# Optimization experiments

Measured on AMD Instinct MI355X. Metric: run time of the kernel, lower is better.

## Reference

```python
import jax, jax.numpy as jnp
import numpy as np

EMB = 1024
HEADS = 16
HEAD_SIZE = EMB // HEADS  # 64
B, T = 2, 2048


def setup_inputs() -> dict:
    key = jax.random.key(0)
    k1, k2, k3 = jax.random.split(key, 3)
    x = jax.random.normal(k1, (B, T, EMB), dtype=jnp.float32)
    # scale weights like typical init to keep logits sane
    w_qkv = jax.random.normal(k2, (EMB, 3 * EMB), dtype=jnp.float32) * (EMB ** -0.5)
    w_proj = jax.random.normal(k3, (EMB, EMB), dtype=jnp.float32) * (EMB ** -0.5)
    b_proj = jnp.zeros((EMB,), dtype=jnp.float32)
    return {"x": x, "w_qkv": w_qkv, "w_proj": w_proj, "b_proj": b_proj}


def reference(x, w_qkv, w_proj, b_proj):
    Bb, Tt, C = x.shape
    qkv = x @ w_qkv  # [B,T,3C]
    q, k, v = jnp.split(qkv, 3, axis=-1)
    # [B,H,T,hs]
    q = q.reshape(Bb, Tt, HEADS, HEAD_SIZE).transpose(0, 2, 1, 3)
    k = k.reshape(Bb, Tt, HEADS, HEAD_SIZE).transpose(0, 2, 1, 3)
    v = v.reshape(Bb, Tt, HEADS, HEAD_SIZE).transpose(0, 2, 1, 3)
    scale = HEAD_SIZE ** -0.5
    wei = jnp.einsum('bhqd,bhkd->bhqk', q, k) * scale  # [B,H,T,T]
    causal = jnp.tril(jnp.ones((Tt, Tt), dtype=bool))
    wei = jnp.where(causal, wei, -jnp.inf)
    wei = jax.nn.softmax(wei, axis=-1)
    out = jnp.einsum('bhqk,bhkd->bhqd', wei, v)  # [B,H,T,hs]
    out = out.transpose(0, 2, 1, 3).reshape(Bb, Tt, C)
    out = out @ w_proj + b_proj
    return out
```

## Files before the change

### kernel.cpp

```cpp
#include <hip/hip_runtime.h>
#include <hip/hip_bf16.h>

typedef __attribute__((ext_vector_type(8))) short short8;
typedef __attribute__((ext_vector_type(4))) float floatx4;

#define MFMA16(a, b, c) __builtin_amdgcn_mfma_f32_16x16x32_bf16((a), (b), (c), 0, 0, 0)
#define GLOBAL_AS __attribute__((address_space(1)))
#define LDS_AS __attribute__((address_space(3)))

__device__ __forceinline__ unsigned short f2bf(float x) {
  union { float f; unsigned u; } v; v.f = x;
  unsigned r = v.u + 0x7FFFu + ((v.u >> 16) & 1u);
  return (unsigned short)(r >> 16);
}

__device__ __forceinline__ short8 ld8(const unsigned short* p) {
  return *reinterpret_cast<const short8*>(p);
}

__device__ __forceinline__ void async_cp16(const unsigned short* g, unsigned short* l) {
  __builtin_amdgcn_global_load_lds((const GLOBAL_AS void*)g, (LDS_AS void*)l, 16, 0, 0);
}

__global__ void k_f32_to_bf16(const float* __restrict__ in,
                              unsigned short* __restrict__ out, int n4) {
  int i = blockIdx.x * blockDim.x + threadIdx.x;
  if (i >= n4) return;
  float4 f = reinterpret_cast<const float4*>(in)[i];
  union { unsigned short u[4]; unsigned long long v; } o;
  o.u[0] = f2bf(f.x); o.u[1] = f2bf(f.y); o.u[2] = f2bf(f.z); o.u[3] = f2bf(f.w);
  reinterpret_cast<unsigned long long*>(out)[i] = o.v;
}

__global__ void k_transpose_bf16(const float* __restrict__ in,
                                 unsigned short* __restrict__ out, int R, int C) {
  __shared__ float tile[64][65];
  int c0 = blockIdx.x * 64, r0 = blockIdx.y * 64;
  int tx = threadIdx.x, ty = threadIdx.y;
  for (int i = ty; i < 64; i += 4)
    tile[i][tx] = in[(size_t)(r0 + i) * C + c0 + tx];
  __syncthreads();
  for (int i = ty; i < 64; i += 4)
    out[(size_t)(c0 + i) * R + r0 + tx] = f2bf(tile[tx][i]);
}

__global__ void k_vtrans(const unsigned short* __restrict__ qkvb,
                         unsigned short* __restrict__ vT) {
  const int T = 2048, LD = 3072;
  __shared__ unsigned short tile[64][72];
  int bh = blockIdx.y, b = bh >> 4, h = bh & 15;
  int t0 = blockIdx.x * 64;
  int tx = threadIdx.x, ty = threadIdx.y;
  const unsigned short* src = qkvb + (size_t)b * T * LD + 2048 + h * 64;
  for (int i = ty; i < 64; i += 4)
    tile[i][tx] = src[(size_t)(t0 + i) * LD + tx];
  __syncthreads();
  unsigned short* dst = vT + (size_t)bh * 64 * T;
  for (int i = ty; i < 64; i += 4)
    dst[(size_t)i * T + t0 + tx] = tile[tx][i];
}

template <int OUT_BF16, int HAS_BIAS>
__global__ __launch_bounds__(256) void k_gemm_bt(
    const unsigned short* __restrict__ A, const unsigned short* __restrict__ Bt,
    void* __restrict__ Cout, const float* __restrict__ bias, int M, int N, int K) {
  __shared__ unsigned short As[128][64];
  __shared__ unsigned short Bs[128][64];
  int tid = threadIdx.x;
  int w = tid >> 6, lane = tid & 63, quad = lane >> 4, l16 = lane & 15;
  int wy = w >> 1, wx = w & 1;
  int rowB = blockIdx.y * 128, colB = blockIdx.x * 128;
  int srcRow = lane >> 3;
  int srcCol = (((lane & 7) ^ (srcRow & 7)) << 3);

  floatx4 acc[4][4];
  floatx4 zero4 = {0.f, 0.f, 0.f, 0.f};
#pragma unroll
  for (int mi = 0; mi < 4; ++mi)
#pragma unroll
    for (int ni = 0; ni < 4; ++ni) acc[mi][ni] = zero4;

  for (int kt = 0; kt < K; kt += 64) {
    __syncthreads();
#pragma unroll
    for (int i = 0; i < 4; ++i) {
      int r0 = w * 32 + i * 8;
      async_cp16(&A[(size_t)(rowB + r0 + srcRow) * K + kt + srcCol], &As[r0][0]);
      async_cp16(&Bt[(size_t)(colB + r0 + srcRow) * K + kt + srcCol], &Bs[r0][0]);
    }
    __syncthreads();
#pragma unroll
    for (int kh = 0; kh < 2; ++kh) {
      short8 af[4], bf_[4];
#pragma unroll
      for (int mi = 0; mi < 4; ++mi)
        af[mi] = ld8(&As[wy * 64 + mi * 16 + l16][((kh * 4 + quad) ^ (l16 & 7)) << 3]);
#pragma unroll
      for (int ni = 0; ni < 4; ++ni)
        bf_[ni] = ld8(&Bs[wx * 64 + ni * 16 + l16][((kh * 4 + quad) ^ (l16 & 7)) << 3]);
#pragma unroll
      for (int mi = 0; mi < 4; ++mi)
#pragma unroll
        for (int ni = 0; ni < 4; ++ni)
          acc[mi][ni] = MFMA16(af[mi], bf_[ni], acc[mi][ni]);
    }
  }

#pragma unroll
  for (int mi = 0; mi < 4; ++mi) {
    int row = rowB + wy * 64 + mi * 16 + quad * 4;
#pragma unroll
    for (int ni = 0; ni < 4; ++ni) {
      int col = colB + wx * 64 + ni * 16 + l16;
      float bv = HAS_BIAS ? bias[col] : 0.f;
#pragma unroll
      for (int r = 0; r < 4; ++r) {
        float val = acc[mi][ni][r] + bv;
        if (OUT_BF16)
          ((unsigned short*)Cout)[(size_t)(row + r) * N + col] = f2bf(val);
        else
          ((float*)Cout)[(size_t)(row + r) * N + col] = val;
      }
    }
  }
}

__global__ __launch_bounds__(256) void k_attn(
    const unsigned short* __restrict__ qkv, const unsigned short* __restrict__ vT,
    unsigned short* __restrict__ attn_out) {
  const int T = 2048, LD = 3072;
  __shared__ unsigned short Kt[64][72];
  __shared__ unsigned short Vt[64][72];
  __shared__ unsigned short Pt[4][2][16][72];

  int bh = blockIdx.y, b = bh >> 4, h = bh & 15;
  int ip = blockIdx.x;
  int tid = threadIdx.x, w = tid >> 6, lane = tid & 63;
  int quad = lane >> 4, l16 = lane & 15;

  const unsigned short* Qp = qkv + (size_t)b * T * LD + h * 64;
  const unsigned short* Kp = Qp + 1024;
  const unsigned short* Vp = vT + (size_t)bh * 64 * T;

  const int q0s[2] = {ip * 64, (31 - ip) * 64};
  const int lastkt[2] = {ip, 31 - ip};
  int nt = 32 - ip;

  short8 aq[2][2];
#pragma unroll
  for (int m = 0; m < 2; ++m) {
    const unsigned short* qrow = Qp + (size_t)(q0s[m] + w * 16 + l16) * LD + quad * 8;
    aq[m][0] = ld8(qrow);
    aq[m][1] = ld8(qrow + 32);
  }

  short8 ones8;
  {
    unsigned short o = 0x3F80;
#pragma unroll
    for (int j = 0; j < 8; ++j) ones8[j] = (short)o;
  }

  const float cscale = 0.125f * 1.44269504f;
  floatx4 o_acc[2][4], l_acc[2];
  floatx4 zero4 = {0.f, 0.f, 0.f, 0.f};
#pragma unroll
  for (int m = 0; m < 2; ++m) {
    l_acc[m] = zero4;
#pragma unroll
    for (int nd = 0; nd < 4; ++nd) o_acc[m][nd] = zero4;
  }

  int stR = tid >> 3, stC = (tid & 7) << 3;

  short8 kreg[2], vreg[2];
#pragma unroll
  for (int j = 0; j < 2; ++j) {
    int r = stR + j * 32;
    kreg[j] = ld8(&Kp[(size_t)r * LD + stC]);
    vreg[j] = ld8(&Vp[(size_t)r * T + stC]);
  }

  for (int kt = 0; kt < nt; ++kt) {
    __syncthreads();
#pragma unroll
    for (int j = 0; j < 2; ++j) {
      int r = stR + j * 32;
      *reinterpret_cast<short8*>(&Kt[r][stC]) = kreg[j];
      *reinterpret_cast<short8*>(&Vt[r][stC]) = vreg[j];
    }
    __syncthreads();

    if (kt + 1 < nt) {
      int key0n = (kt + 1) * 64;
#pragma unroll
      for (int j = 0; j < 2; ++j) {
        int r = stR + j * 32;
        kreg[j] = ld8(&Kp[(size_t)(key0n + r) * LD + stC]);
        vreg[j] = ld8(&Vp[(size_t)r * T + key0n + stC]);
      }
    }

    int key0 = kt * 64;
    bool act0 = (kt <= lastkt[0]);

    floatx4 st[2][4];
#pragma unroll
    for (int kt4 = 0; kt4 < 4; ++kt4) {
      short8 ak0 = ld8(&Kt[kt4 * 16 + l16][quad * 8]);
      short8 ak1 = ld8(&Kt[kt4 * 16 + l16][32 + quad * 8]);
      st[1][kt4] = MFMA16(ak0, aq[1][0], zero4);
      st[1][kt4] = MFMA16(ak1, aq[1][1], st[1][kt4]);
      if (act0) {
        st[0][kt4] = MFMA16(ak0, aq[0][0], zero4);
        st[0][kt4] = MFMA16(ak1, aq[0][1], st[0][kt4]);
      }
    }

#pragma unroll
    for (int m = 0; m < 2; ++m) {
      if (m == 0 && !act0) continue;
      if (kt == lastkt[m]) {
        int qlane = q0s[m] + w * 16 + l16;
#pragma unroll
        for (int kt4 = 0; kt4 < 4; ++kt4)
#pragma unroll
          for (int r = 0; r < 4; ++r)
            if (key0 + kt4 * 16 + quad * 4 + r > qlane) st[m][kt4][r] = -1e30f;
      }
#pragma unroll
      for (int kt4 = 0; kt4 < 4; ++kt4) {
        unsigned u[4];
#pragma unroll
        for (int r = 0; r < 4; ++r)
          u[r] = __float_as_uint(
              __builtin_amdgcn_exp2f(fmaf(st[m][kt4][r], cscale, -16.f)));
        unsigned lo = __builtin_amdgcn_perm(u[1], u[0], 0x07060302u);
        unsigned hi = __builtin_amdgcn_perm(u[3], u[2], 0x07060302u);
        unsigned long long pv = ((unsigned long long)hi << 32) | lo;
        *reinterpret_cast<unsigned long long*>(
            &Pt[w][m][l16][kt4 * 16 + quad * 4]) = pv;
      }
    }

    short8 pa[2][2];
    pa[1][0] = ld8(&Pt[w][1][l16][quad * 8]);
    pa[1][1] = ld8(&Pt[w][1][l16][32 + quad * 8]);
    if (act0) {
      pa[0][0] = ld8(&Pt[w][0][l16][quad * 8]);
      pa[0][1] = ld8(&Pt[w][0][l16][32 + quad * 8]);
    }
#pragma unroll
    for (int nd = 0; nd < 4; ++nd) {
      short8 bv0 = ld8(&Vt[nd * 16 + l16][quad * 8]);
      short8 bv1 = ld8(&Vt[nd * 16 + l16][32 + quad * 8]);
      o_acc[1][nd] = MFMA16(pa[1][0], bv0, o_acc[1][nd]);
      o_acc[1][nd] = MFMA16(pa[1][1], bv1, o_acc[1][nd]);
      if (act0) {
        o_acc[0][nd] = MFMA16(pa[0][0], bv0, o_acc[0][nd]);
        o_acc[0][nd] = MFMA16(pa[0][1], bv1, o_acc[0][nd]);
      }
    }
    l_acc[1] = MFMA16(pa[1][0], ones8, l_acc[1]);
    l_acc[1] = MFMA16(pa[1][1], ones8, l_acc[1]);
    if (act0) {
      l_acc[0] = MFMA16(pa[0][0], ones8, l_acc[0]);
      l_acc[0] = MFMA16(pa[0][1], ones8, l_acc[0]);
    }
  }

#pragma unroll
  for (int m = 0; m < 2; ++m)
#pragma unroll
    for (int nd = 0; nd < 4; ++nd)
#pragma unroll
      for (int r = 0; r < 4; ++r) {
        int q = q0s[m] + w * 16 + quad * 4 + r;
        int d = nd * 16 + l16;
        attn_out[(size_t)(b * T + q) * 1024 + h * 64 + d] =
            f2bf(o_acc[m][nd][r] / l_acc[m][r]);
      }
}

extern "C" void kernel_launch(void* const* d_in, const int* in_sizes, int n_in,
                              void* d_out, int out_size, void* d_ws, size_t ws_size,
                              hipStream_t stream) {
  const float* x = (const float*)d_in[0];
  const float* w_qkv = (const float*)d_in[1];
  const float* w_proj = (const float*)d_in[2];
  const float* b_proj = (const float*)d_in[3];
  float* out = (float*)d_out;

  char* ws = (char*)d_ws;
  unsigned short* xb     = (unsigned short*)(ws);
  unsigned short* wqkvT  = (unsigned short*)(ws + (size_t)(8  << 20));
  unsigned short* wprojT = (unsigned short*)(ws + (size_t)(14 << 20));
  unsigned short* qkvb   = (unsigned short*)(ws + (size_t)(16 << 20));
  unsigned short* attnb  = (unsigned short*)(ws + (size_t)(40 << 20));
  unsigned short* vTb    = xb;

  k_f32_to_bf16<<<4096, 256, 0, stream>>>(x, xb, (4096 * 1024) / 4);
  dim3 tb(64, 4);
  k_transpose_bf16<<<dim3(3072 / 64, 1024 / 64), tb, 0, stream>>>(w_qkv, wqkvT, 1024, 3072);
  k_transpose_bf16<<<dim3(1024 / 64, 1024 / 64), tb, 0, stream>>>(w_proj, wprojT, 1024, 1024);
  k_gemm_bt<1, 0><<<dim3(3072 / 128, 4096 / 128), 256, 0, stream>>>(
      xb, wqkvT, qkvb, nullptr, 4096, 3072, 1024);
  k_vtrans<<<dim3(2048 / 64, 2 * 16), tb, 0, stream>>>(qkvb, vTb);
  k_attn<<<dim3(16, 2 * 16), 256, 0, stream>>>(qkvb, vTb, attnb);
  k_gemm_bt<0, 1><<<dim3(1024 / 128, 4096 / 128), 256, 0, stream>>>(
      attnb, wprojT, out, b_proj, 4096, 1024, 1024);
}
```

Baseline: 200.3 us.

## Double-buffer K/V tiles in LDS to drop one barrier per iteration

Turns the K and V shared-memory tiles into two-slot buffers. Each iteration writes the next tile into the other slot and issues global loads two tiles ahead, so only one __syncthreads per iteration remains. It also pads the P staging rows from 72 to 76 elements, likely to change the LDS bank mapping. The cost is more LDS per block, which may lower occupancy, and a deeper register prefetch.

```diff
diff --git a/kernel.cpp b/kernel.cpp
--- a/kernel.cpp
+++ b/kernel.cpp
@@ -129,9 +129,9 @@
     const unsigned short* __restrict__ qkv, const unsigned short* __restrict__ vT,
     unsigned short* __restrict__ attn_out) {
   const int T = 2048, LD = 3072;
-  __shared__ unsigned short Kt[64][72];
-  __shared__ unsigned short Vt[64][72];
-  __shared__ unsigned short Pt[4][2][16][72];
+  __shared__ unsigned short Kt[2][64][72];
+  __shared__ unsigned short Vt[2][64][72];
+  __shared__ unsigned short Pt[4][2][16][76];
 
   int bh = blockIdx.y, b = bh >> 4, h = bh & 15;
   int ip = blockIdx.x;
@@ -180,24 +180,39 @@
     kreg[j] = ld8(&Kp[(size_t)r * LD + stC]);
     vreg[j] = ld8(&Vp[(size_t)r * T + stC]);
   }
-
-  for (int kt = 0; kt < nt; ++kt) {
-    __syncthreads();
+#pragma unroll
+  for (int j = 0; j < 2; ++j) {
+    int r = stR + j * 32;
+    *reinterpret_cast<short8*>(&Kt[0][r][stC]) = kreg[j];
+    *reinterpret_cast<short8*>(&Vt[0][r][stC]) = vreg[j];
+  }
+  if (nt > 1) {
 #pragma unroll
     for (int j = 0; j < 2; ++j) {
       int r = stR + j * 32;
-      *reinterpret_cast<short8*>(&Kt[r][stC]) = kreg[j];
-      *reinterpret_cast<short8*>(&Vt[r][stC]) = vreg[j];
-    }
-    __syncthreads();
-
+      kreg[j] = ld8(&Kp[(size_t)(64 + r) * LD + stC]);
+      vreg[j] = ld8(&Vp[(size_t)r * T + 64 + stC]);
+    }
+  }
+  __syncthreads();
+
+  for (int kt = 0; kt < nt; ++kt) {
+    int cur = kt & 1;
     if (kt + 1 < nt) {
-      int key0n = (kt + 1) * 64;
 #pragma unroll
       for (int j = 0; j < 2; ++j) {
         int r = stR + j * 32;
-        kreg[j] = ld8(&Kp[(size_t)(key0n + r) * LD + stC]);
-        vreg[j] = ld8(&Vp[(size_t)r * T + key0n + stC]);
+        *reinterpret_cast<short8*>(&Kt[1 - cur][r][stC]) = kreg[j];
+        *reinterpret_cast<short8*>(&Vt[1 - cur][r][stC]) = vreg[j];
+      }
+      if (kt + 2 < nt) {
+        int key0n = (kt + 2) * 64;
+#pragma unroll
+        for (int j = 0; j < 2; ++j) {
+          int r = stR + j * 32;
+          kreg[j] = ld8(&Kp[(size_t)(key0n + r) * LD + stC]);
+          vreg[j] = ld8(&Vp[(size_t)r * T + key0n + stC]);
+        }
       }
     }
 
@@ -207,8 +222,8 @@
     floatx4 st[2][4];
 #pragma unroll
     for (int kt4 = 0; kt4 < 4; ++kt4) {
-      short8 ak0 = ld8(&Kt[kt4 * 16 + l16][quad * 8]);
-      short8 ak1 = ld8(&Kt[kt4 * 16 + l16][32 + quad * 8]);
+      short8 ak0 = ld8(&Kt[cur][kt4 * 16 + l16][quad * 8]);
+      short8 ak1 = ld8(&Kt[cur][kt4 * 16 + l16][32 + quad * 8]);
       st[1][kt4] = MFMA16(ak0, aq[1][0], zero4);
       st[1][kt4] = MFMA16(ak1, aq[1][1], st[1][kt4]);
       if (act0) {
@@ -252,8 +267,8 @@
     }
 #pragma unroll
     for (int nd = 0; nd < 4; ++nd) {
-      short8 bv0 = ld8(&Vt[nd * 16 + l16][quad * 8]);
-      short8 bv1 = ld8(&Vt[nd * 16 + l16][32 + quad * 8]);
+      short8 bv0 = ld8(&Vt[cur][nd * 16 + l16][quad * 8]);
+      short8 bv1 = ld8(&Vt[cur][nd * 16 + l16][32 + quad * 8]);
       o_acc[1][nd] = MFMA16(pa[1][0], bv0, o_acc[1][nd]);
       o_acc[1][nd] = MFMA16(pa[1][1], bv1, o_acc[1][nd]);
       if (act0) {
@@ -267,6 +282,8 @@
       l_acc[0] = MFMA16(pa[0][0], ones8, l_acc[0]);
       l_acc[0] = MFMA16(pa[0][1], ones8, l_acc[0]);
     }
+
+    __syncthreads();
   }
 
 #pragma unroll
```

New measurement: 210.9 us. 5.3% more time.

## Replace paired causal q-block scheduling with one q-block per workgroup

Applied to the files above, without the earlier changes.

The attention kernel previously gave each workgroup two query blocks (ip and 31-ip) so every workgroup did equal causal work while sharing each K/V tile load. It now launches 32 workgroups per head, each handling a single query block, with the heaviest blocks scheduled first via the reversed block index. This doubles parallelism (1024 workgroups instead of 512) and halves per-wave registers, but it loses the K/V reuse across two query blocks, so total K/V loads go up and per-workgroup work becomes unbalanced. The P staging buffer is shrunk and re-padded to 76 columns.

```diff
diff --git a/kernel.cpp b/kernel.cpp
--- a/kernel.cpp
+++ b/kernel.cpp
@@ -131,10 +131,10 @@
   const int T = 2048, LD = 3072;
   __shared__ unsigned short Kt[64][72];
   __shared__ unsigned short Vt[64][72];
-  __shared__ unsigned short Pt[4][2][16][72];
+  __shared__ unsigned short Pt[4][16][76];
 
   int bh = blockIdx.y, b = bh >> 4, h = bh & 15;
-  int ip = blockIdx.x;
+  int qblk = 31 - blockIdx.x;
   int tid = threadIdx.x, w = tid >> 6, lane = tid & 63;
   int quad = lane >> 4, l16 = lane & 15;
 
@@ -142,16 +142,14 @@
   const unsigned short* Kp = Qp + 1024;
   const unsigned short* Vp = vT + (size_t)bh * 64 * T;
 
-  const int q0s[2] = {ip * 64, (31 - ip) * 64};
-  const int lastkt[2] = {ip, 31 - ip};
-  int nt = 32 - ip;
-
-  short8 aq[2][2];
-#pragma unroll
-  for (int m = 0; m < 2; ++m) {
-    const unsigned short* qrow = Qp + (size_t)(q0s[m] + w * 16 + l16) * LD + quad * 8;
-    aq[m][0] = ld8(qrow);
-    aq[m][1] = ld8(qrow + 32);
+  int q0 = qblk * 64;
+  int nt = qblk + 1;
+
+  short8 aq[2];
+  {
+    const unsigned short* qrow = Qp + (size_t)(q0 + w * 16 + l16) * LD + quad * 8;
+    aq[0] = ld8(qrow);
+    aq[1] = ld8(qrow + 32);
   }
 
   short8 ones8;
@@ -162,14 +160,11 @@
   }
 
   const float cscale = 0.125f * 1.44269504f;
-  floatx4 o_acc[2][4], l_acc[2];
+  floatx4 o_acc[4], l_acc;
   floatx4 zero4 = {0.f, 0.f, 0.f, 0.f};
-#pragma unroll
-  for (int m = 0; m < 2; ++m) {
-    l_acc[m] = zero4;
-#pragma unroll
-    for (int nd = 0; nd < 4; ++nd) o_acc[m][nd] = zero4;
-  }
+  l_acc = zero4;
+#pragma unroll
+  for (int nd = 0; nd < 4; ++nd) o_acc[nd] = zero4;
 
   int stR = tid >> 3, stC = (tid & 7) << 3;
 
@@ -202,84 +197,61 @@
     }
 
     int key0 = kt * 64;
-    bool act0 = (kt <= lastkt[0]);
-
-    floatx4 st[2][4];
+
+    floatx4 st[4];
 #pragma unroll
     for (int kt4 = 0; kt4 < 4; ++kt4) {
       short8 ak0 = ld8(&Kt[kt4 * 16 + l16][quad * 8]);
       short8 ak1 = ld8(&Kt[kt4 * 16 + l16][32 + quad * 8]);
-      st[1][kt4] = MFMA16(ak0, aq[1][0], zero4);
-      st[1][kt4] = MFMA16(ak1, aq[1][1], st[1][kt4]);
-      if (act0) {
-        st[0][kt4] = MFMA16(ak0, aq[0][0], zero4);
-        st[0][kt4] = MFMA16(ak1, aq[0][1], st[0][kt4]);
-      }
-    }
-
-#pragma unroll
-    for (int m = 0; m < 2; ++m) {
-      if (m == 0 && !act0) continue;
-      if (kt == lastkt[m]) {
-        int qlane = q0s[m] + w * 16 + l16;
-#pragma unroll
-        for (int kt4 = 0; kt4 < 4; ++kt4)
-#pragma unroll
-          for (int r = 0; r < 4; ++r)
-            if (key0 + kt4 * 16 + quad * 4 + r > qlane) st[m][kt4][r] = -1e30f;
-      }
-#pragma unroll
-      for (int kt4 = 0; kt4 < 4; ++kt4) {
-        unsigned u[4];
+      st[kt4] = MFMA16(ak0, aq[0], zero4);
+      st[kt4] = MFMA16(ak1, aq[1], st[kt4]);
+    }
+
+    if (kt == nt - 1) {
+      int qlane = q0 + w * 16 + l16;
+#pragma unroll
+      for (int kt4 = 0; kt4 < 4; ++kt4)
 #pragma unroll
         for (int r = 0; r < 4; ++r)
-          u[r] = __float_as_uint(
-              __builtin_amdgcn_exp2f(fmaf(st[m][kt4][r], cscale, -16.f)));
-        unsigned lo = __builtin_amdgcn_perm(u[1], u[0], 0x07060302u);
-        unsigned hi = __builtin_amdgcn_perm(u[3], u[2], 0x07060302u);
-        unsigned long long pv = ((unsigned long long)hi << 32) | lo;
-        *reinterpret_cast<unsigned long long*>(
-            &Pt[w][m][l16][kt4 * 16 + quad * 4]) = pv;
-      }
-    }
-
-    short8 pa[2][2];
-    pa[1][0] = ld8(&Pt[w][1][l16][quad * 8]);
-    pa[1][1] = ld8(&Pt[w][1][l16][32 + quad * 8]);
-    if (act0) {
-      pa[0][0] = ld8(&Pt[w][0][l16][quad * 8]);
-      pa[0][1] = ld8(&Pt[w][0][l16][32 + quad * 8]);
-    }
+          if (key0 + kt4 * 16 + quad * 4 + r > qlane) st[kt4][r] = -1e30f;
+    }
+
+#pragma unroll
+    for (int kt4 = 0; kt4 < 4; ++kt4) {
+      unsigned u[4];
+#pragma unroll
+      for (int r = 0; r < 4; ++r)
+        u[r] = __float_as_uint(
+            __builtin_amdgcn_exp2f(fmaf(st[kt4][r], cscale, -16.f)));
+      unsigned lo = __builtin_amdgcn_perm(u[1], u[0], 0x07060302u);
+      unsigned hi = __builtin_amdgcn_perm(u[3], u[2], 0x07060302u);
+      unsigned long long pv = ((unsigned long long)hi << 32) | lo;
+      *reinterpret_cast<unsigned long long*>(
+          &Pt[w][l16][kt4 * 16 + quad * 4]) = pv;
+    }
+
+    short8 pa0 = ld8(&Pt[w][l16][quad * 8]);
+    short8 pa1 = ld8(&Pt[w][l16][32 + quad * 8]);
 #pragma unroll
     for (int nd = 0; nd < 4; ++nd) {
       short8 bv0 = ld8(&Vt[nd * 16 + l16][quad * 8]);
       short8 bv1 = ld8(&Vt[nd * 16 + l16][32 + quad * 8]);
-      o_acc[1][nd] = MFMA16(pa[1][0], bv0, o_acc[1][nd]);
-      o_acc[1][nd] = MFMA16(pa[1][1], bv1, o_acc[1][nd]);
-      if (act0) {
-        o_acc[0][nd] = MFMA16(pa[0][0], bv0, o_acc[0][nd]);
-        o_acc[0][nd] = MFMA16(pa[0][1], bv1, o_acc[0][nd]);
-      }
-    }
-    l_acc[1] = MFMA16(pa[1][0], ones8, l_acc[1]);
-    l_acc[1] = MFMA16(pa[1][1], ones8, l_acc[1]);
-    if (act0) {
-      l_acc[0] = MFMA16(pa[0][0], ones8, l_acc[0]);
-      l_acc[0] = MFMA16(pa[0][1], ones8, l_acc[0]);
-    }
-  }
-
-#pragma unroll
-  for (int m = 0; m < 2; ++m)
-#pragma unroll
-    for (int nd = 0; nd < 4; ++nd)
-#pragma unroll
-      for (int r = 0; r < 4; ++r) {
-        int q = q0s[m] + w * 16 + quad * 4 + r;
-        int d = nd * 16 + l16;
-        attn_out[(size_t)(b * T + q) * 1024 + h * 64 + d] =
-            f2bf(o_acc[m][nd][r] / l_acc[m][r]);
-      }
+      o_acc[nd] = MFMA16(pa0, bv0, o_acc[nd]);
+      o_acc[nd] = MFMA16(pa1, bv1, o_acc[nd]);
+    }
+    l_acc = MFMA16(pa0, ones8, l_acc);
+    l_acc = MFMA16(pa1, ones8, l_acc);
+  }
+
+#pragma unroll
+  for (int nd = 0; nd < 4; ++nd)
+#pragma unroll
+    for (int r = 0; r < 4; ++r) {
+      int q = q0 + w * 16 + quad * 4 + r;
+      int d = nd * 16 + l16;
+      attn_out[(size_t)(b * T + q) * 1024 + h * 64 + d] =
+          f2bf(o_acc[nd][r] / l_acc[r]);
+    }
 }
 
 extern "C" void kernel_launch(void* const* d_in, const int* in_sizes, int n_in,
@@ -306,7 +278,7 @@
   k_gemm_bt<1, 0><<<dim3(3072 / 128, 4096 / 128), 256, 0, stream>>>(
       xb, wqkvT, qkvb, nullptr, 4096, 3072, 1024);
   k_vtrans<<<dim3(2048 / 64, 2 * 16), tb, 0, stream>>>(qkvb, vTb);
-  k_attn<<<dim3(16, 2 * 16), 256, 0, stream>>>(qkvb, vTb, attnb);
+  k_attn<<<dim3(32, 2 * 16), 256, 0, stream>>>(qkvb, vTb, attnb);
   k_gemm_bt<0, 1><<<dim3(1024 / 128, 4096 / 128), 256, 0, stream>>>(
       attnb, wprojT, out, b_proj, 4096, 1024, 1024);
 }
```

After: 226.7 us. 13.2% more time.
